# Optimization experiments

Hardware: AMD Instinct MI355X
Metric: run time of the kernel (lower is better)

## Reference

```python
import jax, jax.numpy as jnp
import numpy as np

TOPK = 13
NUM_CLASSES = 80
ALPHA = 1.0
BETA = 6.0
EPS = 1e-9
BS, NA, NMAX = 16, 8400, 64
IMG = 640


def _anchor_grid():
    pts = []
    for s in (8, 16, 32):
        n = IMG // s
        yv, xv = jnp.meshgrid(jnp.arange(n, dtype=jnp.float32), jnp.arange(n, dtype=jnp.float32), indexing='ij')
        pts.append(jnp.stack([(xv + 0.5) * s, (yv + 0.5) * s], -1).reshape(-1, 2))
    return jnp.concatenate(pts, 0)  # (8400, 2)


def setup_inputs() -> dict:
    key = jax.random.key(0)
    ks = jax.random.split(key, 6)
    pd_scores = jax.nn.sigmoid(jax.random.normal(ks[0], (BS, NA, NUM_CLASSES), jnp.float32))
    # predicted circles: centers in image, radii in [4, 68]
    pxy = jax.random.uniform(ks[1], (BS, NA, 2), jnp.float32) * IMG
    pr = jax.random.uniform(ks[1], (BS, NA, 1), jnp.float32) * 64.0 + 4.0
    pd_circles = jnp.concatenate([pxy, pr], -1)
    anc_points = _anchor_grid()
    gt_labels = jax.random.randint(ks[2], (BS, NMAX, 1), 0, NUM_CLASSES, jnp.int32)
    gxy = jax.random.uniform(ks[3], (BS, NMAX, 2), jnp.float32) * IMG
    gr = jax.random.uniform(ks[3], (BS, NMAX, 1), jnp.float32) * 64.0 + 8.0
    gt_bboxes = jnp.concatenate([gxy, gr], -1)  # circles (x, y, r)
    n_valid = jax.random.randint(ks[4], (BS, 1), 8, NMAX + 1)
    mask_gt = (jnp.arange(NMAX)[None, :] < n_valid).astype(jnp.float32)[..., None]
    return {"pd_scores": pd_scores, "pd_circles": pd_circles, "anc_points": anc_points,
            "gt_labels": gt_labels, "gt_bboxes": gt_bboxes, "mask_gt": mask_gt}


def circle_iou(c1, c2, eps):
    # c1, c2: broadcastable (..., 3) = (x, y, r); IoU of two discs via lens area.
    d = jnp.sqrt(jnp.sum((c1[..., :2] - c2[..., :2]) ** 2, -1) + eps)
    r1, r2 = c1[..., 2], c2[..., 2]
    a1, a2 = jnp.pi * r1 ** 2, jnp.pi * r2 ** 2
    cos1 = jnp.clip((d ** 2 + r1 ** 2 - r2 ** 2) / (2.0 * d * r1 + eps), -1.0, 1.0)
    cos2 = jnp.clip((d ** 2 + r2 ** 2 - r1 ** 2) / (2.0 * d * r2 + eps), -1.0, 1.0)
    tri = jnp.clip((r1 + r2 - d) * (d + r1 - r2) * (d - r1 + r2) * (d + r1 + r2), 0.0)
    lens = r1 ** 2 * jnp.arccos(cos1) + r2 ** 2 * jnp.arccos(cos2) - 0.5 * jnp.sqrt(tri)
    inter = jnp.where(d >= r1 + r2, 0.0,
                      jnp.where(d <= jnp.abs(r1 - r2), jnp.pi * jnp.minimum(r1, r2) ** 2, lens))
    return inter / (a1 + a2 - inter + eps)


def reference(pd_scores, pd_circles, anc_points, gt_labels, gt_bboxes, mask_gt):
    bs, na, nc = pd_scores.shape
    n_max = gt_bboxes.shape[1]
    # ---- candidates inside GT circles: (b, n_max, na) ----
    dist = jnp.linalg.norm(gt_bboxes[:, :, None, :2] - anc_points[None, None, :, :], axis=-1)
    mask_in_gts = (dist <= gt_bboxes[:, :, None, 2]).astype(jnp.float32)
    mask_valid = mask_in_gts * mask_gt  # mask_gt (b, n_max, 1) broadcasts
    # ---- alignment metric ----
    labels = jnp.clip(gt_labels[..., 0], 0, nc - 1)  # (b, n_max)
    b_idx = jnp.arange(bs)[:, None, None]
    a_idx = jnp.arange(na)[None, None, :]
    bbox_scores = pd_scores[b_idx, a_idx, labels[:, :, None]] * mask_valid  # (b, n_max, na)
    overlaps = circle_iou(gt_bboxes[:, :, None, :], pd_circles[:, None, :, :], EPS) * mask_valid
    align_metric = bbox_scores ** ALPHA * overlaps ** BETA
    # ---- topk candidate selection with duplicate suppression ----
    _, topk_idxs = jax.lax.top_k(align_metric, TOPK)  # (b, n_max, TOPK)
    topk_idxs = jnp.where(mask_gt > 0, topk_idxs, 0)
    count = jnp.zeros((bs, n_max, na), jnp.float32).at[
        jnp.arange(bs)[:, None, None], jnp.arange(n_max)[None, :, None], topk_idxs].add(1.0)
    mask_topk = jnp.where(count > 1, 0.0, count)
    mask_pos = mask_topk * mask_in_gts * mask_gt  # (b, n_max, na)
    # ---- resolve anchors claimed by multiple GTs via max overlap ----
    fg_count = mask_pos.sum(1)  # (b, na)
    is_max = jax.nn.one_hot(overlaps.argmax(1), n_max, axis=1, dtype=jnp.float32)  # (b, n_max, na)
    mask_pos = jnp.where(fg_count[:, None, :] > 1, is_max, mask_pos)
    fg_mask = mask_pos.sum(1)  # (b, na)
    target_gt_idx = mask_pos.argmax(1)  # (b, na)
    # ---- gather targets ----
    target_labels = jnp.clip(jnp.take_along_axis(gt_labels[..., 0], target_gt_idx, axis=1), 0, None)
    target_circles = jnp.take_along_axis(gt_bboxes, target_gt_idx[..., None], axis=1)  # (b, na, 3)
    target_scores = jax.nn.one_hot(target_labels, nc, dtype=pd_scores.dtype)
    target_scores = target_scores * (fg_mask[..., None] > 0)
    # ---- normalize scores by aligned metric ----
    align_metric = align_metric * mask_pos
    pos_align = jnp.max(align_metric, -1, keepdims=True)  # (b, n_max, 1)
    pos_overlaps = jnp.max(overlaps * mask_pos, -1, keepdims=True)
    norm = jnp.max(align_metric * pos_overlaps / (pos_align + EPS), 1)[..., None]  # (b, na, 1)
    target_scores = target_scores * norm
    return target_labels, target_circles, target_scores, fg_mask, target_gt_idx
```

## Files before the change

### kernel.cpp

```cpp
#include <hip/hip_runtime.h>
#include <cmath>

#define NA 8400
#define NC 80
#define BS 16
#define NMAX 64
#define TOPKK 13
#define CAP 768
#define CEPS 1e-9f
#define PIF 3.14159265358979323846f

#define OFF_LABELS  0
#define OFF_CIRCLES 134400
#define OFF_SCORES  537600
#define OFF_FG      11289600
#define OFF_TGI     11424000

#define WS_OVKEY   1075200
#define WS_POSAL   2150400
#define WS_POSOV   2154496
#define WS_TGI     2158592
#define WS_ALIGN   2696192
#define ZERO_WS_F4 134912

__device__ __forceinline__ float circle_iou_dev(float gx, float gy, float r1,
                                                float px, float py, float r2) {
    float dx = gx - px, dy = gy - py;
    float d = sqrtf(dx * dx + dy * dy + CEPS);
    float a1 = PIF * r1 * r1, a2 = PIF * r2 * r2;
    float d2 = d * d;
    float c1 = (d2 + r1 * r1 - r2 * r2) / (2.0f * d * r1 + CEPS);
    float c2 = (d2 + r2 * r2 - r1 * r1) / (2.0f * d * r2 + CEPS);
    c1 = fminf(fmaxf(c1, -1.0f), 1.0f);
    c2 = fminf(fmaxf(c2, -1.0f), 1.0f);
    float tri = fmaxf((r1 + r2 - d) * (d + r1 - r2) * (d - r1 + r2) * (d + r1 + r2), 0.0f);
    float lens = r1 * r1 * acosf(c1) + r2 * r2 * acosf(c2) - 0.5f * sqrtf(tri);
    float inter;
    if (d >= r1 + r2)             inter = 0.0f;
    else if (d <= fabsf(r1 - r2)) { float rm = fminf(r1, r2); inter = PIF * rm * rm; }
    else                          inter = lens;
    return inter / (a1 + a2 - inter + CEPS);
}

__global__ __launch_bounds__(256) void k0_zero(float4* __restrict__ wsz)
{
    int i = blockIdx.x * 256 + threadIdx.x;
    if (i < ZERO_WS_F4) wsz[i] = make_float4(0.f, 0.f, 0.f, 0.f);
}

__global__ __launch_bounds__(256) void k1_topk(
    const float* __restrict__ pd_scores, const float* __restrict__ pd_circles,
    const int* __restrict__ gt_labels, const float* __restrict__ gt_bboxes,
    const float* __restrict__ mask_gt, unsigned long long* __restrict__ colbits,
    unsigned long long* __restrict__ ovkey)
{
    __shared__ int   s_cidx[CAP];
    __shared__ float s_cval[CAP];
    __shared__ float s_low[64];
    __shared__ unsigned long long s_ingt0;
    __shared__ int   s_ncand, s_nsel, s_done;
    __shared__ float s_redv[4];
    __shared__ int   s_redi[4], s_redc[4];
    __shared__ int   s_sel[16];

    const int row = blockIdx.x;
    const int b = row >> 6, j = row & 63;
    const int t = threadIdx.x;
    const int lane = t & 63, wv = t >> 6;

    if (mask_gt[row] <= 0.0f) return;

    const float gx = gt_bboxes[row * 3 + 0];
    const float gy = gt_bboxes[row * 3 + 1];
    const float gr = gt_bboxes[row * 3 + 2];
    int lab = gt_labels[row];
    lab = min(max(lab, 0), NC - 1);

    if (t == 0) { s_ncand = 0; s_nsel = 0; s_done = 0; }
    if (t < 64) s_low[t] = 0.0f;
    __syncthreads();

    if (wv == 0) {
        float ax = ((float)lane + 0.5f) * 8.0f, ay = 4.0f;
        float dx = gx - ax, dy = gy - ay;
        bool in0 = (sqrtf(dx * dx + dy * dy) <= gr);
        unsigned long long m = __ballot(in0);
        if (lane == 0) s_ingt0 = m;
    }

    const int strides_[3] = {8, 16, 32};
    const int ns_[3]      = {80, 40, 20};
    const int bases_[3]   = {0, 6400, 8000};
#pragma unroll
    for (int l = 0; l < 3; ++l) {
        const float sl = (float)strides_[l];
        const int n_l = ns_[l], base_l = bases_[l];
        const float inv = 1.0f / sl;
        int y0 = (int)ceilf((gy - gr) * inv - 0.5f) - 1;
        int y1 = (int)floorf((gy + gr) * inv - 0.5f) + 1;
        int x0 = (int)ceilf((gx - gr) * inv - 0.5f) - 1;
        int x1 = (int)floorf((gx + gr) * inv - 0.5f) + 1;
        y0 = max(y0, 0); x0 = max(x0, 0);
        y1 = min(y1, n_l - 1); x1 = min(x1, n_l - 1);
        const int W = x1 - x0 + 1, H = y1 - y0 + 1;
        if (W > 0 && H > 0) {
            const int cells = W * H;
            for (int c = t; c < cells; c += 256) {
                const int q = c / W;
                const int iy = y0 + q, ix = x0 + (c - q * W);
                float ax = ((float)ix + 0.5f) * sl;
                float ay = ((float)iy + 0.5f) * sl;
                float dx = gx - ax, dy = gy - ay;
                if (sqrtf(dx * dx + dy * dy) <= gr) {
                    int p = atomicAdd(&s_ncand, 1);
                    if (p < CAP) s_cidx[p] = base_l + iy * n_l + ix;
                }
            }
        }
    }
    __syncthreads();
    const int n = min(s_ncand, CAP);

    for (int c = t; c < n; c += 256) {
        int a = s_cidx[c];
        size_t pi = (size_t)(b * NA + a);
        float px = pd_circles[pi * 3 + 0];
        float py = pd_circles[pi * 3 + 1];
        float pr = pd_circles[pi * 3 + 2];
        float iou = circle_iou_dev(gx, gy, gr, px, py, pr);
        float sc  = pd_scores[pi * NC + lab];
        float o2 = iou * iou;
        float v = sc * (o2 * o2 * o2);
        s_cval[c] = v;
        if (a < 64) s_low[a] = v;
        unsigned long long key =
            ((unsigned long long)__float_as_uint(iou) << 32) |
            (unsigned long long)(63 - j);
        atomicMax(&ovkey[(size_t)b * NA + a], key);
    }
    __syncthreads();

    for (int it = 0; it < TOPKK; ++it) {
        float bv = -1.0f; int bi = 1 << 30, bc = -1;
        for (int c = t; c < n; c += 256) {
            float v = s_cval[c]; int a = s_cidx[c];
            if (v > bv || (v == bv && a < bi)) { bv = v; bi = a; bc = c; }
        }
        for (int off = 32; off > 0; off >>= 1) {
            float ov = __shfl_down(bv, off);
            int   oi = __shfl_down(bi, off);
            int   oc = __shfl_down(bc, off);
            if (ov > bv || (ov == bv && oi < bi)) { bv = ov; bi = oi; bc = oc; }
        }
        if (lane == 0) { s_redv[wv] = bv; s_redi[wv] = bi; s_redc[wv] = bc; }
        __syncthreads();
        if (t == 0) {
            float vb = s_redv[0]; int ib = s_redi[0], cb = s_redc[0];
            for (int w = 1; w < 4; ++w)
                if (s_redv[w] > vb || (s_redv[w] == vb && s_redi[w] < ib))
                    { vb = s_redv[w]; ib = s_redi[w]; cb = s_redc[w]; }
            if (vb > 0.0f) { s_sel[s_nsel] = ib; s_nsel++; s_cval[cb] = -1.0f; }
            else s_done = 1;
        }
        __syncthreads();
        if (s_done) break;
    }

    if (t == 0) {
        int r = TOPKK - s_nsel;
        if (r > 0) {
            for (int idx = 0; idx < 64 && r > 0; ++idx) {
                if (s_low[idx] > 0.0f) continue;
                r--;
                if ((s_ingt0 >> idx) & 1ull) { s_sel[s_nsel] = idx; s_nsel++; }
            }
        }
    }
    __syncthreads();

    if (t < s_nsel)
        atomicOr(&colbits[(size_t)b * NA + s_sel[t]], 1ull << j);
}

__global__ __launch_bounds__(256) void k2_resolve(
    const float* __restrict__ pd_scores, const float* __restrict__ pd_circles,
    const float* __restrict__ anc, const int* __restrict__ gt_labels,
    const float* __restrict__ gt_bboxes, const float* __restrict__ mask_gt,
    const unsigned long long* __restrict__ colbits,
    const unsigned long long* __restrict__ ovkey,
    float* __restrict__ out, int* __restrict__ tgiE, float* __restrict__ alignv,
    unsigned int* __restrict__ posal, unsigned int* __restrict__ posov)
{
    const int idx = blockIdx.x * 256 + threadIdx.x;
    const int b = idx / NA;
    const int a = idx - b * NA;

    const unsigned long long col = colbits[idx];
    const int cnt = __popcll(col);

    int tgi = 0, fg = 0;
    if (cnt == 1) { fg = 1; tgi = __ffsll((unsigned long long)col) - 1; }
    else if (cnt > 1) {
        fg = 1;
        const unsigned long long key = ovkey[idx];
        const unsigned int ib = (unsigned int)(key >> 32);
        tgi = (ib != 0u) ? (63 - (int)(key & 63ull)) : 0;
    }

    const int gl = gt_labels[b * NMAX + tgi];
    const float gx = gt_bboxes[(b * NMAX + tgi) * 3 + 0];
    const float gy = gt_bboxes[(b * NMAX + tgi) * 3 + 1];
    const float gr = gt_bboxes[(b * NMAX + tgi) * 3 + 2];

    out[OFF_LABELS + idx] = (float)max(gl, 0);
    out[OFF_CIRCLES + (size_t)idx * 3 + 0] = gx;
    out[OFF_CIRCLES + (size_t)idx * 3 + 1] = gy;
    out[OFF_CIRCLES + (size_t)idx * 3 + 2] = gr;
    out[OFF_FG + idx]  = (float)fg;
    out[OFF_TGI + idx] = (float)tgi;
    tgiE[idx] = fg ? tgi : -1;

    float alg = 0.0f;
    if (fg) {
        float ovv = 0.0f;
        float mgv = mask_gt[b * NMAX + tgi];
        float ax = anc[2 * a], ay = anc[2 * a + 1];
        float dx = gx - ax, dy = gy - ay;
        if (mgv > 0.0f && sqrtf(dx * dx + dy * dy) <= gr) {
            float px = pd_circles[(size_t)idx * 3 + 0];
            float py = pd_circles[(size_t)idx * 3 + 1];
            float pr = pd_circles[(size_t)idx * 3 + 2];
            float iou = circle_iou_dev(gx, gy, gr, px, py, pr);
            int lab = min(max(gl, 0), NC - 1);
            float sc = pd_scores[((size_t)b * NA + a) * NC + lab];
            ovv = iou;
            float o2 = iou * iou;
            alg = sc * (o2 * o2 * o2);
        }
        atomicMax(&posal[b * NMAX + tgi], __float_as_uint(alg));
        atomicMax(&posov[b * NMAX + tgi], __float_as_uint(ovv));
    }
    alignv[idx] = alg;
}

__global__ __launch_bounds__(256) void k4_dense(
    const int* __restrict__ tgiE, const float* __restrict__ alignv,
    const unsigned int* __restrict__ posal, const unsigned int* __restrict__ posov,
    const int* __restrict__ gt_labels, float4* __restrict__ scores4)
{
    const int f = blockIdx.x * 256 + threadIdx.x;
    const int a_idx = f / 20;
    const int p = f - a_idx * 20;

    float4 v = make_float4(0.f, 0.f, 0.f, 0.f);
    const int tg = tgiE[a_idx];
    if (tg >= 0) {
        const int b = a_idx / NA;
        const float pa = __uint_as_float(posal[b * NMAX + tg]);
        const float po = __uint_as_float(posov[b * NMAX + tg]);
        const float norm = alignv[a_idx] * po / (pa + CEPS);
        const int lab = max(gt_labels[b * NMAX + tg], 0);
        if ((lab >> 2) == p) ((float*)&v)[lab & 3] = norm;
    }
    scores4[f] = v;
}

extern "C" void kernel_launch(void* const* d_in, const int* in_sizes, int n_in,
                              void* d_out, int out_size, void* d_ws, size_t ws_size,
                              hipStream_t stream) {
    const float* pd_scores  = (const float*)d_in[0];
    const float* pd_circles = (const float*)d_in[1];
    const float* anc        = (const float*)d_in[2];
    const int*   gt_labels  = (const int*)d_in[3];
    const float* gt_bboxes  = (const float*)d_in[4];
    const float* mask_gt    = (const float*)d_in[5];
    float* out = (float*)d_out;

    char* ws = (char*)d_ws;
    unsigned long long* colbits = (unsigned long long*)ws;
    unsigned long long* ovkey   = (unsigned long long*)(ws + WS_OVKEY);
    unsigned int* posal = (unsigned int*)(ws + WS_POSAL);
    unsigned int* posov = (unsigned int*)(ws + WS_POSOV);
    int*   tgiE   = (int*)(ws + WS_TGI);
    float* alignv = (float*)(ws + WS_ALIGN);

    k0_zero<<<(ZERO_WS_F4 + 255) / 256, 256, 0, stream>>>((float4*)ws);
    k1_topk<<<BS * NMAX, 256, 0, stream>>>(pd_scores, pd_circles, gt_labels,
                                           gt_bboxes, mask_gt, colbits, ovkey);
    k2_resolve<<<(BS * NA) / 256, 256, 0, stream>>>(pd_scores, pd_circles, anc,
                                                    gt_labels, gt_bboxes, mask_gt,
                                                    colbits, ovkey, out, tgiE,
                                                    alignv, posal, posov);
    k4_dense<<<(BS * NA * NC / 4) / 256, 256, 0, stream>>>(tgiE, alignv, posal,
                                                           posov, gt_labels,
                                                           (float4*)(out + OFF_SCORES));
}
```

Baseline: 147.3 us.

## Do top-k selection in one wavefront registers and aggregate candidate atomics per wave

The iterative top-13 selection now runs in a single 64-lane wavefront. Candidates are held in registers (12 per lane, covering CAP 768) and reduced with xor shuffles, which removes two block-wide barriers per iteration and the shared-memory reduction. Candidate compaction uses a ballot plus one atomicAdd per wave instead of one LDS atomic per thread. The cost is higher register pressure from the unrolled arrays, and the other three waves sit idle during selection.

```diff
diff --git a/kernel.cpp b/kernel.cpp
--- a/kernel.cpp
+++ b/kernel.cpp
@@ -7,6 +7,7 @@
 #define NMAX 64
 #define TOPKK 13
 #define CAP 768
+#define NN_REG 12
 #define CEPS 1e-9f
 #define PIF 3.14159265358979323846f
 
@@ -57,11 +58,7 @@
     __shared__ int   s_cidx[CAP];
     __shared__ float s_cval[CAP];
     __shared__ float s_low[64];
-    __shared__ unsigned long long s_ingt0;
-    __shared__ int   s_ncand, s_nsel, s_done;
-    __shared__ float s_redv[4];
-    __shared__ int   s_redi[4], s_redc[4];
-    __shared__ int   s_sel[16];
+    __shared__ int   s_ncand;
 
     const int row = blockIdx.x;
     const int b = row >> 6, j = row & 63;
@@ -76,16 +73,15 @@
     int lab = gt_labels[row];
     lab = min(max(lab, 0), NC - 1);
 
-    if (t == 0) { s_ncand = 0; s_nsel = 0; s_done = 0; }
+    if (t == 0) s_ncand = 0;
     if (t < 64) s_low[t] = 0.0f;
     __syncthreads();
 
+    unsigned long long m_ingt0 = 0ull;
     if (wv == 0) {
         float ax = ((float)lane + 0.5f) * 8.0f, ay = 4.0f;
         float dx = gx - ax, dy = gy - ay;
-        bool in0 = (sqrtf(dx * dx + dy * dy) <= gr);
-        unsigned long long m = __ballot(in0);
-        if (lane == 0) s_ingt0 = m;
+        m_ingt0 = __ballot(sqrtf(dx * dx + dy * dy) <= gr);
     }
 
     const int strides_[3] = {8, 16, 32};
@@ -105,15 +101,30 @@
         const int W = x1 - x0 + 1, H = y1 - y0 + 1;
         if (W > 0 && H > 0) {
             const int cells = W * H;
-            for (int c = t; c < cells; c += 256) {
-                const int q = c / W;
-                const int iy = y0 + q, ix = x0 + (c - q * W);
-                float ax = ((float)ix + 0.5f) * sl;
-                float ay = ((float)iy + 0.5f) * sl;
-                float dx = gx - ax, dy = gy - ay;
-                if (sqrtf(dx * dx + dy * dy) <= gr) {
-                    int p = atomicAdd(&s_ncand, 1);
-                    if (p < CAP) s_cidx[p] = base_l + iy * n_l + ix;
+            const int kk = (cells + 255) >> 8;
+            for (int k = 0; k < kk; ++k) {
+                const int c = k * 256 + t;
+                bool found = false; int aidx = 0;
+                if (c < cells) {
+                    const int q = c / W;
+                    const int iy = y0 + q, ix = x0 + (c - q * W);
+                    float ax = ((float)ix + 0.5f) * sl;
+                    float ay = ((float)iy + 0.5f) * sl;
+                    float dx = gx - ax, dy = gy - ay;
+                    found = (sqrtf(dx * dx + dy * dy) <= gr);
+                    aidx = base_l + iy * n_l + ix;
+                }
+                unsigned long long m = __ballot(found);
+                if (m) {
+                    const int cnt = __popcll(m);
+                    const int ldr = __ffsll(m) - 1;
+                    int base = 0;
+                    if (lane == ldr) base = atomicAdd(&s_ncand, cnt);
+                    base = __shfl(base, ldr);
+                    if (found) {
+                        int p = base + __popcll(m & ((1ull << lane) - 1ull));
+                        if (p < CAP) s_cidx[p] = aidx;
+                    }
                 }
             }
         }
@@ -140,46 +151,63 @@
     }
     __syncthreads();
 
+    if (wv != 0) return;
+
+    float rv[NN_REG]; int ri[NN_REG];
+#pragma unroll
+    for (int s = 0; s < NN_REG; ++s) {
+        int c = s * 64 + lane;
+        bool ok = (c < n);
+        rv[s] = ok ? s_cval[c] : -1.0f;
+        ri[s] = ok ? s_cidx[c] : (1 << 30);
+    }
+
+    int selv[TOPKK];
+#pragma unroll
+    for (int s = 0; s < TOPKK; ++s) selv[s] = 0;
+    int nsel = 0;
+
     for (int it = 0; it < TOPKK; ++it) {
-        float bv = -1.0f; int bi = 1 << 30, bc = -1;
-        for (int c = t; c < n; c += 256) {
-            float v = s_cval[c]; int a = s_cidx[c];
-            if (v > bv || (v == bv && a < bi)) { bv = v; bi = a; bc = c; }
+        float bv = -1.0f; int bi = 1 << 30;
+#pragma unroll
+        for (int s = 0; s < NN_REG; ++s)
+            if (rv[s] > bv || (rv[s] == bv && ri[s] < bi)) { bv = rv[s]; bi = ri[s]; }
+        for (int off = 32; off > 0; off >>= 1) {
+            float ov = __shfl_xor(bv, off);
+            int   oi = __shfl_xor(bi, off);
+            if (ov > bv || (ov == bv && oi < bi)) { bv = ov; bi = oi; }
         }
-        for (int off = 32; off > 0; off >>= 1) {
-            float ov = __shfl_down(bv, off);
-            int   oi = __shfl_down(bi, off);
-            int   oc = __shfl_down(bc, off);
-            if (ov > bv || (ov == bv && oi < bi)) { bv = ov; bi = oi; bc = oc; }
-        }
-        if (lane == 0) { s_redv[wv] = bv; s_redi[wv] = bi; s_redc[wv] = bc; }
-        __syncthreads();
-        if (t == 0) {
-            float vb = s_redv[0]; int ib = s_redi[0], cb = s_redc[0];
-            for (int w = 1; w < 4; ++w)
-                if (s_redv[w] > vb || (s_redv[w] == vb && s_redi[w] < ib))
-                    { vb = s_redv[w]; ib = s_redi[w]; cb = s_redc[w]; }
-            if (vb > 0.0f) { s_sel[s_nsel] = ib; s_nsel++; s_cval[cb] = -1.0f; }
-            else s_done = 1;
-        }
-        __syncthreads();
-        if (s_done) break;
-    }
-
-    if (t == 0) {
-        int r = TOPKK - s_nsel;
-        if (r > 0) {
-            for (int idx = 0; idx < 64 && r > 0; ++idx) {
-                if (s_low[idx] > 0.0f) continue;
-                r--;
-                if ((s_ingt0 >> idx) & 1ull) { s_sel[s_nsel] = idx; s_nsel++; }
+        if (bv <= 0.0f) break;
+#pragma unroll
+        for (int s = 0; s < TOPKK; ++s) if (s == nsel) selv[s] = bi;
+        nsel++;
+#pragma unroll
+        for (int s = 0; s < NN_REG; ++s) if (ri[s] == bi) rv[s] = -1.0f;
+    }
+
+    {
+        float lowv = s_low[lane];
+        unsigned long long mpos = __ballot(lowv > 0.0f);
+        unsigned long long zeros = ~mpos;
+        int r = TOPKK - nsel;
+        while (r > 0 && zeros) {
+            int idx = __ffsll(zeros) - 1;
+            zeros &= zeros - 1ull;
+            r--;
+            if ((m_ingt0 >> idx) & 1ull) {
+#pragma unroll
+                for (int s = 0; s < TOPKK; ++s) if (s == nsel) selv[s] = idx;
+                nsel++;
             }
         }
     }
-    __syncthreads();
-
-    if (t < s_nsel)
-        atomicOr(&colbits[(size_t)b * NA + s_sel[t]], 1ull << j);
+
+    if (lane == 0) {
+#pragma unroll
+        for (int s = 0; s < TOPKK; ++s)
+            if (s < nsel)
+                atomicOr(&colbits[(size_t)b * NA + selv[s]], 1ull << j);
+    }
 }
 
 __global__ __launch_bounds__(256) void k2_resolve(
```

Result: slower. 152.8 us (+3.7%).
